# Kernel tuning notes

Hardware: AMD Instinct MI355X
Metric: run time of the kernel (lower is better)

The kernel has to match this reference:

```python
import jax, jax.numpy as jnp
import numpy as np

N = 100000
E = 1600000
IN_DIM = 165
HID = 128
OUT_H = 64  # hidden_dim // 2

def setup_inputs() -> dict:
    key = jax.random.key(0)
    ks = jax.random.split(key, 8)
    x = jax.random.normal(ks[0], (N, IN_DIM), dtype=jnp.float32)
    edge_index = jax.random.randint(ks[1], (2, E), 0, N, dtype=jnp.int64)
    s1 = 1.0 / np.sqrt(IN_DIM)
    s2 = 1.0 / np.sqrt(HID)
    s3 = 1.0 / np.sqrt(OUT_H)
    return {
        "x": x,
        "edge_index": edge_index,
        "W1": jax.random.normal(ks[2], (IN_DIM, HID), dtype=jnp.float32) * s1,
        "b1": jnp.zeros((HID,), jnp.float32),
        "Wg": jax.random.normal(ks[3], (HID, OUT_H), dtype=jnp.float32) * s2,
        "a_src": jax.random.normal(ks[4], (OUT_H,), dtype=jnp.float32) * s3,
        "a_dst": jax.random.normal(ks[5], (OUT_H,), dtype=jnp.float32) * s3,
        "bg": jnp.zeros((OUT_H,), jnp.float32),
        "Wfc": jax.random.normal(ks[6], (OUT_H, 2), dtype=jnp.float32) * s3,
        "bfc": jnp.zeros((2,), jnp.float32),
    }

def _add_self_loops(edge_index, n):
    loops = jnp.arange(n, dtype=edge_index.dtype)
    row = jnp.concatenate([edge_index[0], loops])
    col = jnpp_concat = jnp.concatenate([edge_index[1], loops])
    return row, col

def _gcn_layer(x, row, col, W, b, n):
    deg = jax.ops.segment_sum(jnp.ones_like(col, dtype=x.dtype), col, num_segments=n)
    dinv = jnp.where(deg > 0, jax.lax.rsqrt(deg), 0.0)
    h = x @ W                                   # [N, HID]
    msg = h[row] * (dinv[row] * dinv[col])[:, None]  # [E+N, HID]
    return jax.ops.segment_sum(msg, col, num_segments=n) + b

def _gat_layer(x, row, col, W, a_src, a_dst, b, n):
    # single-head GATConv with self-loops, LeakyReLU(0.2), segment softmax over dst
    h = x @ W                                   # [N, OUT_H]
    e = jax.nn.leaky_relu((h @ a_src)[row] + (h @ a_dst)[col], negative_slope=0.2)
    m = jax.ops.segment_max(e, col, num_segments=n)
    ex = jnp.exp(e - m[col])
    s = jax.ops.segment_sum(ex, col, num_segments=n)
    alpha = ex / s[col]                         # every node has a self-loop => s > 0
    out = jax.ops.segment_sum(alpha[:, None] * h[row], col, num_segments=n)
    return out + b

def reference(x, edge_index, W1, b1, Wg, a_src, a_dst, bg, Wfc, bfc):
    n = x.shape[0]
    row, col = _add_self_loops(edge_index, n)
    h = jax.nn.relu(_gcn_layer(x, row, col, W1, b1, n))
    h = jax.nn.relu(_gat_layer(h, row, col, Wg, a_src, a_dst, bg, n))
    return h @ Wfc + bfc
```

## Files before the change

### kernel.cpp

```cpp
#include <hip/hip_runtime.h>
#include <math.h>

#define NSL 0.2f
#define IN_DIM 165
#define HID 128
#define OUT_H 64
#define NCB_MAX 512
#define EPB 4096

typedef __attribute__((ext_vector_type(8))) short bf16x8;
typedef __attribute__((ext_vector_type(4))) float f32x4;

__device__ inline unsigned pack_bf16(float a, float b) {
    unsigned ua = __float_as_uint(a);
    ua += 0x7FFFu + ((ua >> 16) & 1u);
    unsigned ub = __float_as_uint(b);
    ub += 0x7FFFu + ((ub >> 16) & 1u);
    return (ua >> 16) | (ub & 0xFFFF0000u);
}

__device__ __host__ inline int pcol(int i) {
    int j = i >> 1, odd = i & 1;
    return 32 * (j >> 4) + (j & 15) + 16 * odd;
}

__global__ __launch_bounds__(256) void chist(const int* __restrict__ coli, int E,
                                             int* __restrict__ ghist, int ncb) {
    __shared__ int h[NCB_MAX];
    for (int i = threadIdx.x; i < ncb; i += 256) h[i] = 0;
    __syncthreads();
    int e0 = blockIdx.x * EPB;
    int e1 = min(e0 + EPB, E);
    for (int e = e0 + threadIdx.x; e < e1; e += 256)
        atomicAdd(&h[coli[e] >> 8], 1);
    __syncthreads();
    for (int i = threadIdx.x; i < ncb; i += 256)
        if (h[i]) atomicAdd(&ghist[i], h[i]);
}

__global__ __launch_bounds__(NCB_MAX) void cscan(const int* __restrict__ ghist,
                                                 int* __restrict__ cstart,
                                                 int* __restrict__ gcursor,
                                                 int ncb, int E) {
    __shared__ int tmp[NCB_MAX];
    int tid = threadIdx.x;
    int v = (tid < ncb) ? ghist[tid] : 0;
    tmp[tid] = v;
    __syncthreads();
    for (int off = 1; off < NCB_MAX; off <<= 1) {
        int t = (tid >= off) ? tmp[tid - off] : 0;
        __syncthreads();
        tmp[tid] += t;
        __syncthreads();
    }
    if (tid < ncb) {
        int excl = tmp[tid] - v;
        cstart[tid] = excl;
        gcursor[tid] = excl;
    }
    if (tid == ncb - 1) cstart[ncb] = E;
}

__global__ __launch_bounds__(256) void pass1_scatter(const int* __restrict__ rowi,
                                                     const int* __restrict__ coli, int E,
                                                     int* __restrict__ gcursor,
                                                     unsigned* __restrict__ ebuf, int ncb) {
    __shared__ int hist[NCB_MAX];
    __shared__ int base[NCB_MAX];
    int e0 = blockIdx.x * EPB;
    int e1 = min(e0 + EPB, E);
    for (int i = threadIdx.x; i < ncb; i += 256) hist[i] = 0;
    __syncthreads();
    for (int e = e0 + threadIdx.x; e < e1; e += 256)
        atomicAdd(&hist[coli[e] >> 8], 1);
    __syncthreads();
    for (int i = threadIdx.x; i < ncb; i += 256) {
        int h = hist[i];
        base[i] = h ? atomicAdd(&gcursor[i], h) : 0;
        hist[i] = 0;
    }
    __syncthreads();
    for (int e = e0 + threadIdx.x; e < e1; e += 256) {
        int c = coli[e];
        int cb = c >> 8;
        int rank = atomicAdd(&hist[cb], 1);
        ebuf[base[cb] + rank] = ((unsigned)rowi[e] << 8) | (unsigned)(c & 255);
    }
}

__global__ __launch_bounds__(256) void pass2_all(const unsigned* __restrict__ ebuf,
                                                 const int* __restrict__ cstart,
                                                 int* __restrict__ offsets,
                                                 float* __restrict__ dinv,
                                                 int* __restrict__ csr_src,
                                                 int n, int E) {
    __shared__ int cnt[256];
    __shared__ int scan[256];
    __shared__ int offs[256];
    const int tid = threadIdx.x;
    const int cb = blockIdx.x;
    cnt[tid] = 0;
    __syncthreads();
    int s = cstart[cb], e1 = cstart[cb + 1];
    for (int e = s + tid; e < e1; e += 256)
        atomicAdd(&cnt[ebuf[e] & 255u], 1);
    __syncthreads();
    int v = cnt[tid];
    scan[tid] = v;
    __syncthreads();
#pragma unroll
    for (int off = 1; off < 256; off <<= 1) {
        int t = (tid >= off) ? scan[tid - off] : 0;
        __syncthreads();
        scan[tid] += t;
        __syncthreads();
    }
    int off0 = s + scan[tid] - v;
    offs[tid] = off0;
    int node = (cb << 8) + tid;
    if (node < n) {
        offsets[node] = off0;
        dinv[node] = rsqrtf((float)v + 1.0f);
    }
    if (cb == 0 && tid == 0) offsets[n] = E;
    cnt[tid] = 0;
    __syncthreads();
    for (int e = s + tid; e < e1; e += 256) {
        unsigned u = ebuf[e];
        int local = u & 255u;
        int rank = atomicAdd(&cnt[local], 1);
        csr_src[offs[local] + rank] = (int)(u >> 8);
    }
}

__global__ __launch_bounds__(256) void wprep_all(const float* __restrict__ W1,
                                                 const float* __restrict__ b1,
                                                 const float* __restrict__ Wg,
                                                 const float* __restrict__ bg,
                                                 const float* __restrict__ Wfc,
                                                 uint4* __restrict__ wfrag,
                                                 float* __restrict__ b1p,
                                                 uint4* __restrict__ wg2frag,
                                                 float* __restrict__ bgp,
                                                 float2* __restrict__ wfcp) {
    int idx = blockIdx.x * 256 + threadIdx.x;
    if (idx < 3072) {
        int q = idx & 3, n = (idx >> 2) & 127, c = idx >> 9;
        int k0 = c * 32 + q * 8;
        float f[8];
#pragma unroll
        for (int j = 0; j < 8; j++) {
            int k = k0 + j;
            f[j] = (k < IN_DIM) ? W1[k * 128 + n] : 0.f;
        }
        uint4 u;
        u.x = pack_bf16(f[0], f[1]);
        u.y = pack_bf16(f[2], f[3]);
        u.z = pack_bf16(f[4], f[5]);
        u.w = pack_bf16(f[6], f[7]);
        wfrag[idx] = u;
    } else if (idx < 4096) {
        int i2 = idx - 3072;
        int q = i2 & 3, n = (i2 >> 2) & 63, c = i2 >> 8;
        float f[8];
#pragma unroll
        for (int j = 0; j < 8; j++) {
            int ks = c * 32 + q * 8 + j;
            f[j] = Wg[pcol(ks) * 64 + n];
        }
        uint4 u;
        u.x = pack_bf16(f[0], f[1]);
        u.y = pack_bf16(f[2], f[3]);
        u.z = pack_bf16(f[4], f[5]);
        u.w = pack_bf16(f[6], f[7]);
        wg2frag[i2] = u;
    }
    if (idx < 128) b1p[idx] = b1[pcol(idx)];
    if (idx < 64) {
        int o = pcol(idx);
        bgp[idx] = bg[o];
        wfcp[idx] = make_float2(Wfc[o * 2], Wfc[o * 2 + 1]);
    }
}

__global__ __launch_bounds__(256) void gemm1_mfma(const float* __restrict__ x,
                                                  const uint4* __restrict__ wfrag,
                                                  const float* __restrict__ dinv,
                                                  unsigned char* __restrict__ h1p8,
                                                  float* __restrict__ h1s, int M) {
    const int t = threadIdx.x;
    const int wave = t >> 6;
    const int lane = t & 63;
    const int l16 = lane & 15;
    const int quad = lane >> 4;
    const int rowbase = blockIdx.x * 64 + wave * 16;

    int arow = rowbase + l16;
    if (arow >= M) arow = M - 1;
    const float* xr = x + (size_t)arow * IN_DIM;

    f32x4 acc[8];
#pragma unroll
    for (int nt = 0; nt < 8; nt++) acc[nt] = (f32x4){0.f, 0.f, 0.f, 0.f};

#pragma unroll
    for (int c = 0; c < 6; c++) {
        int k0 = c * 32 + quad * 8;
        float f[8];
#pragma unroll
        for (int j = 0; j < 8; j++)
            f[j] = (k0 + j < IN_DIM) ? xr[k0 + j] : 0.f;
        uint4 au;
        au.x = pack_bf16(f[0], f[1]);
        au.y = pack_bf16(f[2], f[3]);
        au.z = pack_bf16(f[4], f[5]);
        au.w = pack_bf16(f[6], f[7]);
        bf16x8 a = __builtin_bit_cast(bf16x8, au);
#pragma unroll
        for (int nt = 0; nt < 8; nt++) {
            uint4 bu = wfrag[(size_t)((c * 128 + nt * 16 + l16) * 4 + quad)];
            bf16x8 b = __builtin_bit_cast(bf16x8, bu);
            acc[nt] = __builtin_amdgcn_mfma_f32_16x16x32_bf16(a, b, acc[nt], 0, 0, 0);
        }
    }

#pragma unroll
    for (int r = 0; r < 4; r++) {
        int row = rowbase + quad * 4 + r;
        if (row < M) {
            float s = dinv[row];
            float v[8];
#pragma unroll
            for (int nt = 0; nt < 8; nt++) v[nt] = acc[nt][r] * s;
            float gm = fabsf(v[0]);
#pragma unroll
            for (int nt = 1; nt < 8; nt++) gm = fmaxf(gm, fabsf(v[nt]));
            gm = fmaxf(gm, __shfl_xor(gm, 1, 16));
            gm = fmaxf(gm, __shfl_xor(gm, 2, 16));
            gm = fmaxf(gm, __shfl_xor(gm, 4, 16));
            gm = fmaxf(gm, __shfl_xor(gm, 8, 16));
            float inv = gm > 0.f ? 127.0f / gm : 0.f;
            unsigned short* hr = (unsigned short*)(h1p8 + (size_t)row * 128);
#pragma unroll
            for (int p = 0; p < 4; p++) {
                int q0 = (int)rintf(v[2 * p] * inv);
                int q1 = (int)rintf(v[2 * p + 1] * inv);
                hr[p * 16 + l16] = (unsigned short)((q0 & 0xff) | ((q1 & 0xff) << 8));
            }
            if (l16 == 0) h1s[row] = gm * (1.0f / 127.0f);
        }
    }
}

__device__ inline void acc8(float* a, uint4 u) {
    a[0] += __uint_as_float(u.x << 16);
    a[1] += __uint_as_float(u.x & 0xFFFF0000u);
    a[2] += __uint_as_float(u.y << 16);
    a[3] += __uint_as_float(u.y & 0xFFFF0000u);
    a[4] += __uint_as_float(u.z << 16);
    a[5] += __uint_as_float(u.z & 0xFFFF0000u);
    a[6] += __uint_as_float(u.w << 16);
    a[7] += __uint_as_float(u.w & 0xFFFF0000u);
}

__device__ inline void fma8i8(float* a, uint2 u, float s) {
    a[0] = fmaf((float)(char)(u.x), s, a[0]);
    a[1] = fmaf((float)(char)(u.x >> 8), s, a[1]);
    a[2] = fmaf((float)(char)(u.x >> 16), s, a[2]);
    a[3] = fmaf((float)(char)(u.x >> 24), s, a[3]);
    a[4] = fmaf((float)(char)(u.y), s, a[4]);
    a[5] = fmaf((float)(char)(u.y >> 8), s, a[5]);
    a[6] = fmaf((float)(char)(u.y >> 16), s, a[6]);
    a[7] = fmaf((float)(char)(u.y >> 24), s, a[7]);
}

__device__ inline void fma8(float* a, uint4 u, float w) {
    a[0] = fmaf(__uint_as_float(u.x << 16), w, a[0]);
    a[1] = fmaf(__uint_as_float(u.x & 0xFFFF0000u), w, a[1]);
    a[2] = fmaf(__uint_as_float(u.y << 16), w, a[2]);
    a[3] = fmaf(__uint_as_float(u.y & 0xFFFF0000u), w, a[3]);
    a[4] = fmaf(__uint_as_float(u.z << 16), w, a[4]);
    a[5] = fmaf(__uint_as_float(u.z & 0xFFFF0000u), w, a[5]);
    a[6] = fmaf(__uint_as_float(u.w << 16), w, a[6]);
    a[7] = fmaf(__uint_as_float(u.w & 0xFFFF0000u), w, a[7]);
}

__device__ inline float lexp(float e) {
    e = e > 0.f ? e : NSL * e;
    return __expf(e);
}

__global__ __launch_bounds__(256) void gcn_gather(const int* __restrict__ offsets,
                                                  const int* __restrict__ csr_src,
                                                  const uint2* __restrict__ h1v8,
                                                  const float* __restrict__ h1s,
                                                  const float* __restrict__ dinv,
                                                  const float* __restrict__ b1p,
                                                  uint4* __restrict__ gb, int n) {
    int node = (blockIdx.x * 256 + threadIdx.x) >> 4;
    int lane = threadIdx.x & 15;
    if (node >= n) return;
    int s0 = offsets[node], s1 = offsets[node + 1];

    float a0[8], a1[8], a2[8], a3[8];
#pragma unroll
    for (int i = 0; i < 8; i++) { a0[i] = 0.f; a1[i] = 0.f; a2[i] = 0.f; a3[i] = 0.f; }
    fma8i8(a0, h1v8[(size_t)node * 16 + lane], h1s[node]);

    int k = s0;
    if (s1 - k >= 4) {
        int r0 = csr_src[k], r1 = csr_src[k + 1], r2 = csr_src[k + 2], r3 = csr_src[k + 3];
        uint2 v0 = h1v8[(size_t)r0 * 16 + lane];
        uint2 v1 = h1v8[(size_t)r1 * 16 + lane];
        uint2 v2 = h1v8[(size_t)r2 * 16 + lane];
        uint2 v3 = h1v8[(size_t)r3 * 16 + lane];
        float w0 = h1s[r0], w1 = h1s[r1], w2 = h1s[r2], w3 = h1s[r3];
        k += 4;
        while (s1 - k >= 4) {
            int q0 = csr_src[k], q1 = csr_src[k + 1], q2 = csr_src[k + 2], q3 = csr_src[k + 3];
            uint2 u0 = h1v8[(size_t)q0 * 16 + lane];
            uint2 u1 = h1v8[(size_t)q1 * 16 + lane];
            uint2 u2 = h1v8[(size_t)q2 * 16 + lane];
            uint2 u3 = h1v8[(size_t)q3 * 16 + lane];
            float y0 = h1s[q0], y1 = h1s[q1], y2 = h1s[q2], y3 = h1s[q3];
            k += 4;
            fma8i8(a0, v0, w0);
            fma8i8(a1, v1, w1);
            fma8i8(a2, v2, w2);
            fma8i8(a3, v3, w3);
            v0 = u0; v1 = u1; v2 = u2; v3 = u3;
            w0 = y0; w1 = y1; w2 = y2; w3 = y3;
        }
        fma8i8(a0, v0, w0);
        fma8i8(a1, v1, w1);
        fma8i8(a2, v2, w2);
        fma8i8(a3, v3, w3);
    }
    for (; k < s1; k++) {
        int r = csr_src[k];
        fma8i8(a0, h1v8[(size_t)r * 16 + lane], h1s[r]);
    }

    float dc = dinv[node];
    float4 bb0 = ((const float4*)b1p)[lane * 2];
    float4 bb1 = ((const float4*)b1p)[lane * 2 + 1];
    float o[8];
    o[0] = fmaxf(((a0[0] + a1[0]) + (a2[0] + a3[0])) * dc + bb0.x, 0.f);
    o[1] = fmaxf(((a0[1] + a1[1]) + (a2[1] + a3[1])) * dc + bb0.y, 0.f);
    o[2] = fmaxf(((a0[2] + a1[2]) + (a2[2] + a3[2])) * dc + bb0.z, 0.f);
    o[3] = fmaxf(((a0[3] + a1[3]) + (a2[3] + a3[3])) * dc + bb0.w, 0.f);
    o[4] = fmaxf(((a0[4] + a1[4]) + (a2[4] + a3[4])) * dc + bb1.x, 0.f);
    o[5] = fmaxf(((a0[5] + a1[5]) + (a2[5] + a3[5])) * dc + bb1.y, 0.f);
    o[6] = fmaxf(((a0[6] + a1[6]) + (a2[6] + a3[6])) * dc + bb1.z, 0.f);
    o[7] = fmaxf(((a0[7] + a1[7]) + (a2[7] + a3[7])) * dc + bb1.w, 0.f);
    uint4 pk;
    pk.x = pack_bf16(o[0], o[1]);
    pk.y = pack_bf16(o[2], o[3]);
    pk.z = pack_bf16(o[4], o[5]);
    pk.w = pack_bf16(o[6], o[7]);
    gb[(size_t)node * 16 + lane] = pk;
}

__global__ __launch_bounds__(256) void gemm2_mfma(const uint4* __restrict__ gb4,
                                                  const uint4* __restrict__ wg2frag,
                                                  const float* __restrict__ a_src,
                                                  const float* __restrict__ a_dst,
                                                  unsigned* __restrict__ h2b,
                                                  float* __restrict__ es,
                                                  float* __restrict__ ed, int M) {
    const int t = threadIdx.x;
    const int wave = t >> 6;
    const int lane = t & 63;
    const int l16 = lane & 15;
    const int quad = lane >> 4;
    const int rowbase = blockIdx.x * 64 + wave * 16;

    int arow = rowbase + l16;
    if (arow >= M) arow = M - 1;

    f32x4 acc[4];
#pragma unroll
    for (int nt = 0; nt < 4; nt++) acc[nt] = (f32x4){0.f, 0.f, 0.f, 0.f};

#pragma unroll
    for (int c = 0; c < 4; c++) {
        uint4 au = gb4[(size_t)arow * 16 + c * 4 + quad];
        bf16x8 a = __builtin_bit_cast(bf16x8, au);
#pragma unroll
        for (int nt = 0; nt < 4; nt++) {
            uint4 bu = wg2frag[(size_t)((c * 64 + nt * 16 + l16) * 4 + quad)];
            bf16x8 b = __builtin_bit_cast(bf16x8, bu);
            acc[nt] = __builtin_amdgcn_mfma_f32_16x16x32_bf16(a, b, acc[nt], 0, 0, 0);
        }
    }

    float as0 = a_src[l16], as1 = a_src[16 + l16], as2 = a_src[32 + l16], as3 = a_src[48 + l16];
    float ad0 = a_dst[l16], ad1 = a_dst[16 + l16], ad2 = a_dst[32 + l16], ad3 = a_dst[48 + l16];

#pragma unroll
    for (int r = 0; r < 4; r++) {
        int row = rowbase + quad * 4 + r;
        float ps = acc[0][r] * as0 + acc[1][r] * as1 + acc[2][r] * as2 + acc[3][r] * as3;
        float pd = acc[0][r] * ad0 + acc[1][r] * ad1 + acc[2][r] * ad2 + acc[3][r] * ad3;
#pragma unroll
        for (int m = 8; m; m >>= 1) {
            ps += __shfl_xor(ps, m, 16);
            pd += __shfl_xor(pd, m, 16);
        }
        if (row < M) {
            h2b[(size_t)row * 32 + l16]      = pack_bf16(acc[0][r], acc[1][r]);
            h2b[(size_t)row * 32 + 16 + l16] = pack_bf16(acc[2][r], acc[3][r]);
            if (l16 == 0) { es[row] = ps; ed[row] = pd; }
        }
    }
}

__global__ __launch_bounds__(256) void gat_fused(const int* __restrict__ offsets,
                                                 const int* __restrict__ csr_src,
                                                 const uint4* __restrict__ h2v,
                                                 const float* __restrict__ es,
                                                 const float* __restrict__ ed,
                                                 const float* __restrict__ bgp,
                                                 const float2* __restrict__ wfcp,
                                                 const float* __restrict__ bfc,
                                                 float* __restrict__ out, int n) {
    int node = (blockIdx.x * 256 + threadIdx.x) >> 3;
    int lane = threadIdx.x & 7;
    if (node >= n) return;
    int s0 = offsets[node], s1 = offsets[node + 1];
    float edc = ed[node];

    float x0s = lexp(es[node] + edc);
    float sA = x0s, sB = 0.f, sC = 0.f, sD = 0.f;
    float aA[8], aB[8], aC[8], aD[8];
#pragma unroll
    for (int i = 0; i < 8; i++) { aA[i] = 0.f; aB[i] = 0.f; aC[i] = 0.f; aD[i] = 0.f; }
    fma8(aA, h2v[(size_t)node * 8 + lane], x0s);

    int k = s0;
    if (s1 - k >= 4) {
        int r0 = csr_src[k], r1 = csr_src[k + 1], r2 = csr_src[k + 2], r3 = csr_src[k + 3];
        float e0 = es[r0], e1 = es[r1], e2 = es[r2], e3 = es[r3];
        uint4 v0 = h2v[(size_t)r0 * 8 + lane];
        uint4 v1 = h2v[(size_t)r1 * 8 + lane];
        uint4 v2 = h2v[(size_t)r2 * 8 + lane];
        uint4 v3 = h2v[(size_t)r3 * 8 + lane];
        k += 4;
        while (s1 - k >= 4) {
            int q0 = csr_src[k], q1 = csr_src[k + 1], q2 = csr_src[k + 2], q3 = csr_src[k + 3];
            float f0 = es[q0], f1 = es[q1], f2 = es[q2], f3 = es[q3];
            uint4 u0 = h2v[(size_t)q0 * 8 + lane];
            uint4 u1 = h2v[(size_t)q1 * 8 + lane];
            uint4 u2 = h2v[(size_t)q2 * 8 + lane];
            uint4 u3 = h2v[(size_t)q3 * 8 + lane];
            k += 4;
            float x0 = lexp(e0 + edc), x1 = lexp(e1 + edc);
            float x2 = lexp(e2 + edc), x3 = lexp(e3 + edc);
            sA += x0; sB += x1; sC += x2; sD += x3;
            fma8(aA, v0, x0);
            fma8(aB, v1, x1);
            fma8(aC, v2, x2);
            fma8(aD, v3, x3);
            e0 = f0; e1 = f1; e2 = f2; e3 = f3;
            v0 = u0; v1 = u1; v2 = u2; v3 = u3;
        }
        float x0 = lexp(e0 + edc), x1 = lexp(e1 + edc);
        float x2 = lexp(e2 + edc), x3 = lexp(e3 + edc);
        sA += x0; sB += x1; sC += x2; sD += x3;
        fma8(aA, v0, x0);
        fma8(aB, v1, x1);
        fma8(aC, v2, x2);
        fma8(aD, v3, x3);
    }
    for (; k < s1; k++) {
        int r = csr_src[k];
        float xv = lexp(es[r] + edc);
        sA += xv;
        fma8(aA, h2v[(size_t)r * 8 + lane], xv);
    }
    float s = (sA + sB) + (sC + sD);
    float rcp = 1.0f / s;
    float4 b0 = ((const float4*)bgp)[lane * 2];
    float4 b1 = ((const float4*)bgp)[lane * 2 + 1];
    float o[8];
    o[0] = fmaxf(((aA[0] + aB[0]) + (aC[0] + aD[0])) * rcp + b0.x, 0.f);
    o[1] = fmaxf(((aA[1] + aB[1]) + (aC[1] + aD[1])) * rcp + b0.y, 0.f);
    o[2] = fmaxf(((aA[2] + aB[2]) + (aC[2] + aD[2])) * rcp + b0.z, 0.f);
    o[3] = fmaxf(((aA[3] + aB[3]) + (aC[3] + aD[3])) * rcp + b0.w, 0.f);
    o[4] = fmaxf(((aA[4] + aB[4]) + (aC[4] + aD[4])) * rcp + b1.x, 0.f);
    o[5] = fmaxf(((aA[5] + aB[5]) + (aC[5] + aD[5])) * rcp + b1.y, 0.f);
    o[6] = fmaxf(((aA[6] + aB[6]) + (aC[6] + aD[6])) * rcp + b1.z, 0.f);
    o[7] = fmaxf(((aA[7] + aB[7]) + (aC[7] + aD[7])) * rcp + b1.w, 0.f);

    float p0 = 0.f, p1 = 0.f;
#pragma unroll
    for (int m2 = 0; m2 < 4; m2++) {
        float4 w = ((const float4*)wfcp)[lane * 4 + m2];
        p0 += o[2 * m2] * w.x + o[2 * m2 + 1] * w.z;
        p1 += o[2 * m2] * w.y + o[2 * m2 + 1] * w.w;
    }
#pragma unroll
    for (int m = 4; m; m >>= 1) {
        p0 += __shfl_xor(p0, m, 8);
        p1 += __shfl_xor(p1, m, 8);
    }
    if (lane == 0) {
        out[(size_t)node * 2 + 0] = p0 + bfc[0];
        out[(size_t)node * 2 + 1] = p1 + bfc[1];
    }
}

extern "C" void kernel_launch(void* const* d_in, const int* in_sizes, int n_in,
                              void* d_out, int out_size, void* d_ws, size_t ws_size,
                              hipStream_t stream) {
    const float* x     = (const float*)d_in[0];
    const int*   ei    = (const int*)d_in[1];
    const float* W1    = (const float*)d_in[2];
    const float* b1    = (const float*)d_in[3];
    const float* Wg    = (const float*)d_in[4];
    const float* a_src = (const float*)d_in[5];
    const float* a_dst = (const float*)d_in[6];
    const float* bg    = (const float*)d_in[7];
    const float* Wfc   = (const float*)d_in[8];
    const float* bfc   = (const float*)d_in[9];
    float* out = (float*)d_out;

    const int N = in_sizes[0] / IN_DIM;
    const int E = in_sizes[1] / 2;
    const int* rowi = ei;
    const int* coli = ei + E;
    const int ncb = (N + 255) >> 8;

    auto alignup = [](char* p) { return (char*)(((uintptr_t)p + 15) & ~(uintptr_t)15); };

    char* wsb = (char*)d_ws;
    int*   offsets = (int*)wsb;
    float* dinv    = (float*)(offsets + N + 8);
    float* es      = dinv + N;
    float* ed      = es + N;
    float* h1s     = ed + N;
    int*   ghist   = (int*)(h1s + N);
    int*   cstart  = ghist + NCB_MAX;
    int*   gcursor = cstart + NCB_MAX + 2;
    float* b1p     = (float*)(gcursor + NCB_MAX);
    float* bgp     = b1p + 128;
    float2* wfcp   = (float2*)(bgp + 64);
    uint4* wfrag   = (uint4*)alignup((char*)(wfcp + 64));
    uint4* wg2frag = wfrag + 3072;
    int*   csr_src = (int*)(wg2frag + 1024);
    unsigned* ebuf = (unsigned*)(csr_src + E);
    unsigned char* h1p8 = (unsigned char*)alignup((char*)(ebuf + E));
    uint4* gb      = (uint4*)alignup((char*)(h1p8 + (size_t)N * 128));
    unsigned* h2b  = (unsigned*)h1p8;

    hipMemsetAsync(ghist, 0, NCB_MAX * 4, stream);

    const int nbE = (E + EPB - 1) / EPB;

    chist<<<nbE, 256, 0, stream>>>(coli, E, ghist, ncb);
    cscan<<<1, NCB_MAX, 0, stream>>>(ghist, cstart, gcursor, ncb, E);
    pass1_scatter<<<nbE, 256, 0, stream>>>(rowi, coli, E, gcursor, ebuf, ncb);
    pass2_all<<<ncb, 256, 0, stream>>>(ebuf, cstart, offsets, dinv, csr_src, N, E);

    wprep_all<<<16, 256, 0, stream>>>(W1, b1, Wg, bg, Wfc, wfrag, b1p, wg2frag, bgp, wfcp);

    gemm1_mfma<<<(N + 63) / 64, 256, 0, stream>>>(x, wfrag, dinv, h1p8, h1s, N);

    gcn_gather<<<(N + 15) / 16, 256, 0, stream>>>(offsets, csr_src, (const uint2*)h1p8,
                                                  h1s, dinv, b1p, gb, N);

    gemm2_mfma<<<(N + 63) / 64, 256, 0, stream>>>(gb, wg2frag, a_src, a_dst, h2b, es, ed, N);

    gat_fused<<<(N + 31) / 32, 256, 0, stream>>>(offsets, csr_src, (const uint4*)h2b,
                                                 es, ed, bgp, wfcp, bfc, out, N);
}
```

Baseline: 329.8 us.

## Bucket CSR edges by source range and gather in synchronized source-bucket phases

Result: slower. 397.7 us (+20.6%).

```diff
diff --git a/kernel.cpp b/kernel.cpp
--- a/kernel.cpp
+++ b/kernel.cpp
@@ -7,6 +7,9 @@
 #define OUT_H 64
 #define NCB_MAX 512
 #define EPB 4096
+#define NB 4
+#define NPQ 9
+#define NPG 5
 
 typedef __attribute__((ext_vector_type(8))) short bf16x8;
 typedef __attribute__((ext_vector_type(4))) float f32x4;
@@ -91,45 +94,59 @@
 __global__ __launch_bounds__(256) void pass2_all(const unsigned* __restrict__ ebuf,
                                                  const int* __restrict__ cstart,
                                                  int* __restrict__ offsets,
+                                                 int* __restrict__ offsets2,
                                                  float* __restrict__ dinv,
                                                  int* __restrict__ csr_src,
                                                  int n, int E) {
-    __shared__ int cnt[256];
-    __shared__ int scan[256];
-    __shared__ int offs[256];
+    __shared__ int cnt[1024];
+    __shared__ int kb[1024];
+    __shared__ int scn[256];
     const int tid = threadIdx.x;
     const int cb = blockIdx.x;
-    cnt[tid] = 0;
+#pragma unroll
+    for (int j = 0; j < 4; j++) cnt[tid * 4 + j] = 0;
     __syncthreads();
     int s = cstart[cb], e1 = cstart[cb + 1];
-    for (int e = s + tid; e < e1; e += 256)
-        atomicAdd(&cnt[ebuf[e] & 255u], 1);
-    __syncthreads();
-    int v = cnt[tid];
-    scan[tid] = v;
+    for (int e = s + tid; e < e1; e += 256) {
+        unsigned u = ebuf[e];
+        int key = ((u & 255u) << 2) | ((u >> 23) & 3u);
+        atomicAdd(&cnt[key], 1);
+    }
+    __syncthreads();
+    int c0 = cnt[tid * 4], c1 = cnt[tid * 4 + 1], c2 = cnt[tid * 4 + 2], c3 = cnt[tid * 4 + 3];
+    int v = c0 + c1 + c2 + c3;
+    scn[tid] = v;
     __syncthreads();
 #pragma unroll
     for (int off = 1; off < 256; off <<= 1) {
-        int t = (tid >= off) ? scan[tid - off] : 0;
+        int t = (tid >= off) ? scn[tid - off] : 0;
         __syncthreads();
-        scan[tid] += t;
+        scn[tid] += t;
         __syncthreads();
     }
-    int off0 = s + scan[tid] - v;
-    offs[tid] = off0;
+    int base = s + scn[tid] - v;
+    kb[tid * 4]     = base;
+    kb[tid * 4 + 1] = base + c0;
+    kb[tid * 4 + 2] = base + c0 + c1;
+    kb[tid * 4 + 3] = base + c0 + c1 + c2;
     int node = (cb << 8) + tid;
     if (node < n) {
-        offsets[node] = off0;
+        offsets[node] = base;
+        offsets2[node * 4]     = base;
+        offsets2[node * 4 + 1] = base + c0;
+        offsets2[node * 4 + 2] = base + c0 + c1;
+        offsets2[node * 4 + 3] = base + c0 + c1 + c2;
         dinv[node] = rsqrtf((float)v + 1.0f);
     }
-    if (cb == 0 && tid == 0) offsets[n] = E;
-    cnt[tid] = 0;
+    if (cb == 0 && tid == 0) { offsets[n] = E; offsets2[4 * n] = E; }
+#pragma unroll
+    for (int j = 0; j < 4; j++) cnt[tid * 4 + j] = 0;
     __syncthreads();
     for (int e = s + tid; e < e1; e += 256) {
         unsigned u = ebuf[e];
-        int local = u & 255u;
-        int rank = atomicAdd(&cnt[local], 1);
-        csr_src[offs[local] + rank] = (int)(u >> 8);
+        int key = ((u & 255u) << 2) | ((u >> 23) & 3u);
+        int rank = atomicAdd(&cnt[key], 1);
+        csr_src[kb[key] + rank] = (int)(u >> 8);
     }
 }
 
@@ -252,17 +269,6 @@
     }
 }
 
-__device__ inline void acc8(float* a, uint4 u) {
-    a[0] += __uint_as_float(u.x << 16);
-    a[1] += __uint_as_float(u.x & 0xFFFF0000u);
-    a[2] += __uint_as_float(u.y << 16);
-    a[3] += __uint_as_float(u.y & 0xFFFF0000u);
-    a[4] += __uint_as_float(u.z << 16);
-    a[5] += __uint_as_float(u.z & 0xFFFF0000u);
-    a[6] += __uint_as_float(u.w << 16);
-    a[7] += __uint_as_float(u.w & 0xFFFF0000u);
-}
-
 __device__ inline void fma8i8(float* a, uint2 u, float s) {
     a[0] = fmaf((float)(char)(u.x), s, a[0]);
     a[1] = fmaf((float)(char)(u.x >> 8), s, a[1]);
@@ -290,75 +296,79 @@
     return __expf(e);
 }
 
-__global__ __launch_bounds__(256) void gcn_gather(const int* __restrict__ offsets,
-                                                  const int* __restrict__ csr_src,
-                                                  const uint2* __restrict__ h1v8,
-                                                  const float* __restrict__ h1s,
-                                                  const float* __restrict__ dinv,
-                                                  const float* __restrict__ b1p,
-                                                  uint4* __restrict__ gb, int n) {
-    int node = (blockIdx.x * 256 + threadIdx.x) >> 4;
+__global__ __launch_bounds__(256, 3) void gcn_gather(const int* __restrict__ offsets2,
+                                                     const int* __restrict__ csr_src,
+                                                     const uint2* __restrict__ h1v8,
+                                                     const float* __restrict__ h1s,
+                                                     const float* __restrict__ dinv,
+                                                     const float* __restrict__ b1p,
+                                                     uint4* __restrict__ gb,
+                                                     int totq, int n) {
+    int qid = (blockIdx.x << 4) + (threadIdx.x >> 4);
     int lane = threadIdx.x & 15;
-    if (node >= n) return;
-    int s0 = offsets[node], s1 = offsets[node + 1];
-
-    float a0[8], a1[8], a2[8], a3[8];
-#pragma unroll
-    for (int i = 0; i < 8; i++) { a0[i] = 0.f; a1[i] = 0.f; a2[i] = 0.f; a3[i] = 0.f; }
-    fma8i8(a0, h1v8[(size_t)node * 16 + lane], h1s[node]);
-
-    int k = s0;
-    if (s1 - k >= 4) {
-        int r0 = csr_src[k], r1 = csr_src[k + 1], r2 = csr_src[k + 2], r3 = csr_src[k + 3];
-        uint2 v0 = h1v8[(size_t)r0 * 16 + lane];
-        uint2 v1 = h1v8[(size_t)r1 * 16 + lane];
-        uint2 v2 = h1v8[(size_t)r2 * 16 + lane];
-        uint2 v3 = h1v8[(size_t)r3 * 16 + lane];
-        float w0 = h1s[r0], w1 = h1s[r1], w2 = h1s[r2], w3 = h1s[r3];
-        k += 4;
-        while (s1 - k >= 4) {
-            int q0 = csr_src[k], q1 = csr_src[k + 1], q2 = csr_src[k + 2], q3 = csr_src[k + 3];
-            uint2 u0 = h1v8[(size_t)q0 * 16 + lane];
-            uint2 u1 = h1v8[(size_t)q1 * 16 + lane];
-            uint2 u2 = h1v8[(size_t)q2 * 16 + lane];
-            uint2 u3 = h1v8[(size_t)q3 * 16 + lane];
-            float y0 = h1s[q0], y1 = h1s[q1], y2 = h1s[q2], y3 = h1s[q3];
-            k += 4;
-            fma8i8(a0, v0, w0);
-            fma8i8(a1, v1, w1);
-            fma8i8(a2, v2, w2);
-            fma8i8(a3, v3, w3);
-            v0 = u0; v1 = u1; v2 = u2; v3 = u3;
-            w0 = y0; w1 = y1; w2 = y2; w3 = y3;
-        }
-        fma8i8(a0, v0, w0);
-        fma8i8(a1, v1, w1);
-        fma8i8(a2, v2, w2);
-        fma8i8(a3, v3, w3);
-    }
-    for (; k < s1; k++) {
-        int r = csr_src[k];
-        fma8i8(a0, h1v8[(size_t)r * 16 + lane], h1s[r]);
-    }
-
-    float dc = dinv[node];
-    float4 bb0 = ((const float4*)b1p)[lane * 2];
-    float4 bb1 = ((const float4*)b1p)[lane * 2 + 1];
-    float o[8];
-    o[0] = fmaxf(((a0[0] + a1[0]) + (a2[0] + a3[0])) * dc + bb0.x, 0.f);
-    o[1] = fmaxf(((a0[1] + a1[1]) + (a2[1] + a3[1])) * dc + bb0.y, 0.f);
-    o[2] = fmaxf(((a0[2] + a1[2]) + (a2[2] + a3[2])) * dc + bb0.z, 0.f);
-    o[3] = fmaxf(((a0[3] + a1[3]) + (a2[3] + a3[3])) * dc + bb0.w, 0.f);
-    o[4] = fmaxf(((a0[4] + a1[4]) + (a2[4] + a3[4])) * dc + bb1.x, 0.f);
-    o[5] = fmaxf(((a0[5] + a1[5]) + (a2[5] + a3[5])) * dc + bb1.y, 0.f);
-    o[6] = fmaxf(((a0[6] + a1[6]) + (a2[6] + a3[6])) * dc + bb1.z, 0.f);
-    o[7] = fmaxf(((a0[7] + a1[7]) + (a2[7] + a3[7])) * dc + bb1.w, 0.f);
-    uint4 pk;
-    pk.x = pack_bf16(o[0], o[1]);
-    pk.y = pack_bf16(o[2], o[3]);
-    pk.z = pack_bf16(o[4], o[5]);
-    pk.w = pack_bf16(o[6], o[7]);
-    gb[(size_t)node * 16 + lane] = pk;
+    int nstart = (int)((long long)qid * n / totq);
+    int nend   = (int)((long long)(qid + 1) * n / totq);
+
+    float acc[NPQ][8];
+#pragma unroll
+    for (int i = 0; i < NPQ; i++)
+#pragma unroll
+        for (int j = 0; j < 8; j++) acc[i][j] = 0.f;
+
+    for (int b = 0; b < NB; b++) {
+#pragma unroll
+        for (int i = 0; i < NPQ; i++) {
+            int node = nstart + i;
+            if (node < nend) {
+                int k  = offsets2[(node << 2) | b];
+                int e1 = offsets2[((node << 2) | b) + 1];
+                for (; k + 4 <= e1; k += 4) {
+                    int r0 = csr_src[k], r1 = csr_src[k + 1];
+                    int r2 = csr_src[k + 2], r3 = csr_src[k + 3];
+                    uint2 v0 = h1v8[(size_t)r0 * 16 + lane];
+                    uint2 v1 = h1v8[(size_t)r1 * 16 + lane];
+                    uint2 v2 = h1v8[(size_t)r2 * 16 + lane];
+                    uint2 v3 = h1v8[(size_t)r3 * 16 + lane];
+                    float w0 = h1s[r0], w1 = h1s[r1], w2 = h1s[r2], w3 = h1s[r3];
+                    fma8i8(acc[i], v0, w0);
+                    fma8i8(acc[i], v1, w1);
+                    fma8i8(acc[i], v2, w2);
+                    fma8i8(acc[i], v3, w3);
+                }
+                for (; k < e1; k++) {
+                    int r = csr_src[k];
+                    fma8i8(acc[i], h1v8[(size_t)r * 16 + lane], h1s[r]);
+                }
+            }
+        }
+        __syncthreads();
+    }
+
+#pragma unroll
+    for (int i = 0; i < NPQ; i++) {
+        int node = nstart + i;
+        if (node < nend) {
+            fma8i8(acc[i], h1v8[(size_t)node * 16 + lane], h1s[node]);
+            float dc = dinv[node];
+            float4 bb0 = ((const float4*)b1p)[lane * 2];
+            float4 bb1 = ((const float4*)b1p)[lane * 2 + 1];
+            float o[8];
+            o[0] = fmaxf(acc[i][0] * dc + bb0.x, 0.f);
+            o[1] = fmaxf(acc[i][1] * dc + bb0.y, 0.f);
+            o[2] = fmaxf(acc[i][2] * dc + bb0.z, 0.f);
+            o[3] = fmaxf(acc[i][3] * dc + bb0.w, 0.f);
+            o[4] = fmaxf(acc[i][4] * dc + bb1.x, 0.f);
+            o[5] = fmaxf(acc[i][5] * dc + bb1.y, 0.f);
+            o[6] = fmaxf(acc[i][6] * dc + bb1.z, 0.f);
+            o[7] = fmaxf(acc[i][7] * dc + bb1.w, 0.f);
+            uint4 pk;
+            pk.x = pack_bf16(o[0], o[1]);
+            pk.y = pack_bf16(o[2], o[3]);
+            pk.z = pack_bf16(o[4], o[5]);
+            pk.w = pack_bf16(o[6], o[7]);
+            gb[(size_t)node * 16 + lane] = pk;
+        }
+    }
 }
 
 __global__ __launch_bounds__(256) void gemm2_mfma(const uint4* __restrict__ gb4,
@@ -415,98 +425,104 @@
     }
 }
 
-__global__ __launch_bounds__(256) void gat_fused(const int* __restrict__ offsets,
-                                                 const int* __restrict__ csr_src,
-                                                 const uint4* __restrict__ h2v,
-                                                 const float* __restrict__ es,
-                                                 const float* __restrict__ ed,
-                                                 const float* __restrict__ bgp,
-                                                 const float2* __restrict__ wfcp,
-                                                 const float* __restrict__ bfc,
-                                                 float* __restrict__ out, int n) {
-    int node = (blockIdx.x * 256 + threadIdx.x) >> 3;
+__global__ __launch_bounds__(256, 3) void gat_fused(const int* __restrict__ offsets2,
+                                                    const int* __restrict__ csr_src,
+                                                    const uint4* __restrict__ h2v,
+                                                    const float* __restrict__ es,
+                                                    const float* __restrict__ ed,
+                                                    const float* __restrict__ bgp,
+                                                    const float2* __restrict__ wfcp,
+                                                    const float* __restrict__ bfc,
+                                                    float* __restrict__ out,
+                                                    int totq, int n) {
+    int qid = (blockIdx.x << 5) + (threadIdx.x >> 3);
     int lane = threadIdx.x & 7;
-    if (node >= n) return;
-    int s0 = offsets[node], s1 = offsets[node + 1];
-    float edc = ed[node];
-
-    float x0s = lexp(es[node] + edc);
-    float sA = x0s, sB = 0.f, sC = 0.f, sD = 0.f;
-    float aA[8], aB[8], aC[8], aD[8];
-#pragma unroll
-    for (int i = 0; i < 8; i++) { aA[i] = 0.f; aB[i] = 0.f; aC[i] = 0.f; aD[i] = 0.f; }
-    fma8(aA, h2v[(size_t)node * 8 + lane], x0s);
-
-    int k = s0;
-    if (s1 - k >= 4) {
-        int r0 = csr_src[k], r1 = csr_src[k + 1], r2 = csr_src[k + 2], r3 = csr_src[k + 3];
-        float e0 = es[r0], e1 = es[r1], e2 = es[r2], e3 = es[r3];
-        uint4 v0 = h2v[(size_t)r0 * 8 + lane];
-        uint4 v1 = h2v[(size_t)r1 * 8 + lane];
-        uint4 v2 = h2v[(size_t)r2 * 8 + lane];
-        uint4 v3 = h2v[(size_t)r3 * 8 + lane];
-        k += 4;
-        while (s1 - k >= 4) {
-            int q0 = csr_src[k], q1 = csr_src[k + 1], q2 = csr_src[k + 2], q3 = csr_src[k + 3];
-            float f0 = es[q0], f1 = es[q1], f2 = es[q2], f3 = es[q3];
-            uint4 u0 = h2v[(size_t)q0 * 8 + lane];
-            uint4 u1 = h2v[(size_t)q1 * 8 + lane];
-            uint4 u2 = h2v[(size_t)q2 * 8 + lane];
-            uint4 u3 = h2v[(size_t)q3 * 8 + lane];
-            k += 4;
-            float x0 = lexp(e0 + edc), x1 = lexp(e1 + edc);
-            float x2 = lexp(e2 + edc), x3 = lexp(e3 + edc);
-            sA += x0; sB += x1; sC += x2; sD += x3;
-            fma8(aA, v0, x0);
-            fma8(aB, v1, x1);
-            fma8(aC, v2, x2);
-            fma8(aD, v3, x3);
-            e0 = f0; e1 = f1; e2 = f2; e3 = f3;
-            v0 = u0; v1 = u1; v2 = u2; v3 = u3;
-        }
-        float x0 = lexp(e0 + edc), x1 = lexp(e1 + edc);
-        float x2 = lexp(e2 + edc), x3 = lexp(e3 + edc);
-        sA += x0; sB += x1; sC += x2; sD += x3;
-        fma8(aA, v0, x0);
-        fma8(aB, v1, x1);
-        fma8(aC, v2, x2);
-        fma8(aD, v3, x3);
-    }
-    for (; k < s1; k++) {
-        int r = csr_src[k];
-        float xv = lexp(es[r] + edc);
-        sA += xv;
-        fma8(aA, h2v[(size_t)r * 8 + lane], xv);
-    }
-    float s = (sA + sB) + (sC + sD);
-    float rcp = 1.0f / s;
-    float4 b0 = ((const float4*)bgp)[lane * 2];
-    float4 b1 = ((const float4*)bgp)[lane * 2 + 1];
-    float o[8];
-    o[0] = fmaxf(((aA[0] + aB[0]) + (aC[0] + aD[0])) * rcp + b0.x, 0.f);
-    o[1] = fmaxf(((aA[1] + aB[1]) + (aC[1] + aD[1])) * rcp + b0.y, 0.f);
-    o[2] = fmaxf(((aA[2] + aB[2]) + (aC[2] + aD[2])) * rcp + b0.z, 0.f);
-    o[3] = fmaxf(((aA[3] + aB[3]) + (aC[3] + aD[3])) * rcp + b0.w, 0.f);
-    o[4] = fmaxf(((aA[4] + aB[4]) + (aC[4] + aD[4])) * rcp + b1.x, 0.f);
-    o[5] = fmaxf(((aA[5] + aB[5]) + (aC[5] + aD[5])) * rcp + b1.y, 0.f);
-    o[6] = fmaxf(((aA[6] + aB[6]) + (aC[6] + aD[6])) * rcp + b1.z, 0.f);
-    o[7] = fmaxf(((aA[7] + aB[7]) + (aC[7] + aD[7])) * rcp + b1.w, 0.f);
-
-    float p0 = 0.f, p1 = 0.f;
-#pragma unroll
-    for (int m2 = 0; m2 < 4; m2++) {
-        float4 w = ((const float4*)wfcp)[lane * 4 + m2];
-        p0 += o[2 * m2] * w.x + o[2 * m2 + 1] * w.z;
-        p1 += o[2 * m2] * w.y + o[2 * m2 + 1] * w.w;
-    }
-#pragma unroll
-    for (int m = 4; m; m >>= 1) {
-        p0 += __shfl_xor(p0, m, 8);
-        p1 += __shfl_xor(p1, m, 8);
-    }
-    if (lane == 0) {
-        out[(size_t)node * 2 + 0] = p0 + bfc[0];
-        out[(size_t)node * 2 + 1] = p1 + bfc[1];
+    int nstart = (int)((long long)qid * n / totq);
+    int nend   = (int)((long long)(qid + 1) * n / totq);
+
+    float acc[NPG][8];
+    float ssum[NPG];
+    float edc[NPG];
+#pragma unroll
+    for (int i = 0; i < NPG; i++) {
+        ssum[i] = 0.f;
+        int node = nstart + i;
+        edc[i] = (node < nend) ? ed[node] : 0.f;
+#pragma unroll
+        for (int j = 0; j < 8; j++) acc[i][j] = 0.f;
+    }
+
+    for (int b = 0; b < NB; b++) {
+#pragma unroll
+        for (int i = 0; i < NPG; i++) {
+            int node = nstart + i;
+            if (node < nend) {
+                int k  = offsets2[(node << 2) | b];
+                int e1 = offsets2[((node << 2) | b) + 1];
+                float ec = edc[i];
+                for (; k + 4 <= e1; k += 4) {
+                    int r0 = csr_src[k], r1 = csr_src[k + 1];
+                    int r2 = csr_src[k + 2], r3 = csr_src[k + 3];
+                    float e0 = es[r0], e1f = es[r1], e2 = es[r2], e3 = es[r3];
+                    uint4 v0 = h2v[(size_t)r0 * 8 + lane];
+                    uint4 v1 = h2v[(size_t)r1 * 8 + lane];
+                    uint4 v2 = h2v[(size_t)r2 * 8 + lane];
+                    uint4 v3 = h2v[(size_t)r3 * 8 + lane];
+                    float x0 = lexp(e0 + ec), x1 = lexp(e1f + ec);
+                    float x2 = lexp(e2 + ec), x3 = lexp(e3 + ec);
+                    ssum[i] += (x0 + x1) + (x2 + x3);
+                    fma8(acc[i], v0, x0);
+                    fma8(acc[i], v1, x1);
+                    fma8(acc[i], v2, x2);
+                    fma8(acc[i], v3, x3);
+                }
+                for (; k < e1; k++) {
+                    int r = csr_src[k];
+                    float xv = lexp(es[r] + ec);
+                    ssum[i] += xv;
+                    fma8(acc[i], h2v[(size_t)r * 8 + lane], xv);
+                }
+            }
+        }
+        __syncthreads();
+    }
+
+#pragma unroll
+    for (int i = 0; i < NPG; i++) {
+        int node = nstart + i;
+        if (node < nend) {
+            float x0s = lexp(es[node] + edc[i]);
+            fma8(acc[i], h2v[(size_t)node * 8 + lane], x0s);
+            float rcp = 1.0f / (ssum[i] + x0s);
+            float4 b0 = ((const float4*)bgp)[lane * 2];
+            float4 b1 = ((const float4*)bgp)[lane * 2 + 1];
+            float o[8];
+            o[0] = fmaxf(acc[i][0] * rcp + b0.x, 0.f);
+            o[1] = fmaxf(acc[i][1] * rcp + b0.y, 0.f);
+            o[2] = fmaxf(acc[i][2] * rcp + b0.z, 0.f);
+            o[3] = fmaxf(acc[i][3] * rcp + b0.w, 0.f);
+            o[4] = fmaxf(acc[i][4] * rcp + b1.x, 0.f);
+            o[5] = fmaxf(acc[i][5] * rcp + b1.y, 0.f);
+            o[6] = fmaxf(acc[i][6] * rcp + b1.z, 0.f);
+            o[7] = fmaxf(acc[i][7] * rcp + b1.w, 0.f);
+
+            float p0 = 0.f, p1 = 0.f;
+#pragma unroll
+            for (int m2 = 0; m2 < 4; m2++) {
+                float4 w = ((const float4*)wfcp)[lane * 4 + m2];
+                p0 += o[2 * m2] * w.x + o[2 * m2 + 1] * w.z;
+                p1 += o[2 * m2] * w.y + o[2 * m2 + 1] * w.w;
+            }
+#pragma unroll
+            for (int m = 4; m; m >>= 1) {
+                p0 += __shfl_xor(p0, m, 8);
+                p1 += __shfl_xor(p1, m, 8);
+            }
+            if (lane == 0) {
+                out[(size_t)node * 2 + 0] = p0 + bfc[0];
+                out[(size_t)node * 2 + 1] = p1 + bfc[1];
+            }
+        }
     }
 }
 
@@ -534,8 +550,9 @@
     auto alignup = [](char* p) { return (char*)(((uintptr_t)p + 15) & ~(uintptr_t)15); };
 
     char* wsb = (char*)d_ws;
-    int*   offsets = (int*)wsb;
-    float* dinv    = (float*)(offsets + N + 8);
+    int*   offsets  = (int*)wsb;
+    int*   offsets2 = offsets + N + 8;
+    float* dinv    = (float*)(offsets2 + 4 * N + 8);
     float* es      = dinv + N;
     float* ed      = es + N;
     float* h1s     = ed + N;
@@ -560,17 +577,21 @@
     chist<<<nbE, 256, 0, stream>>>(coli, E, ghist, ncb);
     cscan<<<1, NCB_MAX, 0, stream>>>(ghist, cstart, gcursor, ncb, E);
     pass1_scatter<<<nbE, 256, 0, stream>>>(rowi, coli, E, gcursor, ebuf, ncb);
-    pass2_all<<<ncb, 256, 0, stream>>>(ebuf, cstart, offsets, dinv, csr_src, N, E);
+    pass2_all<<<ncb, 256, 0, stream>>>(ebuf, cstart, offsets, offsets2, dinv, csr_src, N, E);
 
     wprep_all<<<16, 256, 0, stream>>>(W1, b1, Wg, bg, Wfc, wfrag, b1p, wg2frag, bgp, wfcp);
 
     gemm1_mfma<<<(N + 63) / 64, 256, 0, stream>>>(x, wfrag, dinv, h1p8, h1s, N);
 
-    gcn_gather<<<(N + 15) / 16, 256, 0, stream>>>(offsets, csr_src, (const uint2*)h1p8,
-                                                  h1s, dinv, b1p, gb, N);
+    int gblocks = 768;
+    while ((long long)gblocks * 16 * NPQ < (long long)N) gblocks += 256;
+    gcn_gather<<<gblocks, 256, 0, stream>>>(offsets2, csr_src, (const uint2*)h1p8,
+                                            h1s, dinv, b1p, gb, gblocks * 16, N);
 
     gemm2_mfma<<<(N + 63) / 64, 256, 0, stream>>>(gb, wg2frag, a_src, a_dst, h2b, es, ed, N);
 
-    gat_fused<<<(N + 31) / 32, 256, 0, stream>>>(offsets, csr_src, (const uint4*)h2b,
-                                                 es, ed, bgp, wfcp, bfc, out, N);
-}
+    int ablocks = 768;
+    while ((long long)ablocks * 32 * NPG < (long long)N) ablocks += 256;
+    gat_fused<<<ablocks, 256, 0, stream>>>(offsets2, csr_src, (const uint4*)h2b,
+                                           es, ed, bgp, wfcp, bfc, out, ablocks * 32, N);
+}
```
